# Kernel tuning notes

Hardware: AMD Instinct MI355X
Metric: run time of the kernel (lower is better)

The kernel has to match this reference:

```python
import jax, jax.numpy as jnp
import numpy as np

N, C, T, V, K = 32, 256, 64, 25, 3   # batch, in_channels, frames, joints, adjacency partitions
D = 256                               # out_channels
KT = 9                                # temporal kernel size
PAD = (KT - 1) // 2
EPS = 1e-5                            # BatchNorm eps (torch default)


def setup_inputs() -> dict:
    key = jax.random.key(0)
    ks = jax.random.split(key, 5)
    x = jax.random.normal(ks[0], (N, C, T, V), jnp.float32)
    A = jax.random.uniform(ks[1], (K, V, V), jnp.float32)           # learnable adjacency
    W_gcn = jax.random.normal(ks[2], (K, D, C), jnp.float32) * (2.0 / C) ** 0.5  # K stacked 1x1 convs
    b_gcn = jnp.zeros((K, D), jnp.float32)
    W_tcn = jax.random.normal(ks[3], (D, D, KT, 1), jnp.float32) * (2.0 / (D * KT)) ** 0.5  # kaiming fan_out
    b_tcn = jnp.zeros((D,), jnp.float32)
    gamma = jnp.ones((D,), jnp.float32)   # bn_init(bn, 1)
    beta = jnp.zeros((D,), jnp.float32)
    return dict(x=x, A=A, W_gcn=W_gcn, b_gcn=b_gcn, W_tcn=W_tcn,
                b_tcn=b_tcn, gamma=gamma, beta=beta)


def reference(x, A, W_gcn, b_gcn, W_tcn, b_tcn, gamma, beta):
    # ---- GCN: per-partition 1x1 conv over channels, then graph aggregation via A[k], summed over k ----
    # y[k,n,d,t,v] = sum_c W_gcn[k,d,c] * x[n,c,t,v] + b_gcn[k,d]
    y = jnp.einsum('kdc,nctv->kndtv', W_gcn, x) + b_gcn[:, None, :, None, None]
    # aggregate neighbors: sum_v y[k,n,d,t,v] * A[k,v,w], accumulated over partitions k
    y = jnp.einsum('kndtv,kvw->ndtw', y, A)        # [N, D, T, V]

    # ---- TCN: (9,1) temporal conv + BatchNorm2d (batch statistics) ----
    z = jax.lax.conv_general_dilated(
        y, W_tcn, window_strides=(1, 1), padding=((PAD, PAD), (0, 0)),
        dimension_numbers=('NCHW', 'OIHW', 'NCHW'))
    z = z + b_tcn[None, :, None, None]
    mean = jnp.mean(z, axis=(0, 2, 3), keepdims=True)
    var = jnp.mean((z - mean) ** 2, axis=(0, 2, 3), keepdims=True)  # biased, as torch BN training fwd
    z = gamma[None, :, None, None] * (z - mean) * jax.lax.rsqrt(var + EPS) + beta[None, :, None, None]

    # ---- residual (identity branch: in==out, stride==1) + ReLU ----
    return jax.nn.relu(z + x)
```

## Files before the change

### kernel.cpp

```cpp
#include <hip/hip_runtime.h>
#include <math.h>

typedef unsigned short u16;
typedef short v8s __attribute__((ext_vector_type(8)));
typedef float v4f __attribute__((ext_vector_type(4)));

#define AS1 __attribute__((address_space(1)))
#define AS3 __attribute__((address_space(3)))

__device__ __forceinline__ float bf2f(u16 u) {
    union { unsigned int i; float f; } c; c.i = ((unsigned int)u) << 16; return c.f;
}
__device__ __forceinline__ u16 f2bf(float f) {
    union { float f; unsigned int i; } c; c.f = f;
    unsigned int u = c.i;
    return (u16)((u + 0x7FFFu + ((u >> 16) & 1u)) >> 16);
}
__device__ __forceinline__ void gload_lds16(const void* g, void* l) {
    __builtin_amdgcn_global_load_lds((const AS1 void*)(uintptr_t)g,
                                     (AS3 void*)(unsigned int)(uintptr_t)l,
                                     16, 0, 0);
}

#define Nn 32
#define Tt 64
#define Vv 25
#define NP 51200
#define NBLK 400

__global__ __launch_bounds__(256) void prep_kernel(
    const float* __restrict__ Wg, const float* __restrict__ Wt,
    const float* __restrict__ A, const float* __restrict__ bg,
    u16* __restrict__ Wgb, u16* __restrict__ Wtb,
    float* __restrict__ bias2, float* __restrict__ zpad)
{
    const int idx = blockIdx.x * 256 + threadIdx.x;
    const int stride = gridDim.x * 256;
    for (int i = idx; i < 256 * 2304; i += stride) {
        int d = i / 2304, r = i - d * 2304, dt = r >> 8, c = r & 255;
        Wtb[i] = f2bf(Wt[(d * 256 + c) * 9 + dt]);
    }
    for (int i = idx; i < 256 * 768; i += stride) {
        int d = i / 768, r = i - d * 768, k = r >> 8, c = r & 255;
        Wgb[i] = f2bf(Wg[(k * 256 + d) * 256 + c]);
    }
    for (int i = idx; i < 25 * 256; i += stride) {
        int w = i >> 8, d = i & 255;
        float s = 0.f;
        for (int k = 0; k < 3; ++k) {
            float cs = 0.f;
            for (int v = 0; v < 25; ++v) cs += A[(k * 25 + v) * 25 + w];
            s += bg[k * 256 + d] * cs;
        }
        bias2[i] = s;
    }
    for (int i = idx; i < 256; i += stride) zpad[i] = 0.f;
}

__global__ __launch_bounds__(256) void xa_kernel(
    const float* __restrict__ x, const float* __restrict__ A,
    u16* __restrict__ xa2)
{
    const int t = blockIdx.x, n = blockIdx.y;
    const int tid = threadIdx.x;
    __shared__ float xs[256 * 25];

    for (int i = tid; i < 6400; i += 256) {
        int c = i / 25, v = i - c * 25;
        xs[i] = x[((n * 256 + c) * 64 + t) * 25 + v];
    }
    __syncthreads();

    float xr[25];
    #pragma unroll
    for (int v = 0; v < 25; ++v) xr[v] = xs[tid * 25 + v];

    const size_t pbase = ((size_t)n * 64 + t) * 25;
    #pragma unroll 1
    for (int k = 0; k < 3; ++k) {
        float o[25];
        #pragma unroll
        for (int w = 0; w < 25; ++w) {
            float acc = 0.f;
            #pragma unroll
            for (int v = 0; v < 25; ++v)
                acc = fmaf(xr[v], A[(k * 25 + v) * 25 + w], acc);
            o[w] = acc;
        }
        u16* dst = xa2 + k * 256 + tid;
        #pragma unroll
        for (int w = 0; w < 25; ++w)
            dst[(pbase + w) * 768] = f2bf(o[w]);
    }
}

template<int KTOT, bool TCN>
__global__ __launch_bounds__(512, 2) void gemm_kernel(
    const u16* __restrict__ Ad, const u16* __restrict__ Bw,
    const float* __restrict__ bias, u16* __restrict__ outB,
    float* __restrict__ psum, float* __restrict__ psq,
    const u16* __restrict__ zpad)
{
    __shared__ u16 smem[24576];
    u16* As = smem;
    u16* Bs = smem + 8192;

    const int tid = threadIdx.x;
    const int wid = tid >> 6, lane = tid & 63;
    const int lr = lane & 15, hk = lane >> 4;
    const int wm = wid >> 2, wn = wid & 3;
    const int blk = blockIdx.x;
    const int rA = lane >> 3, sA = lane & 7;

    v4f acc[4][4];
    const v4f vzero = {0.f, 0.f, 0.f, 0.f};
    #pragma unroll
    for (int mf = 0; mf < 4; ++mf)
        #pragma unroll
        for (int nf = 0; nf < 4; ++nf) acc[mf][nf] = vzero;

    for (int kt = 0; kt < KTOT / 64; ++kt) {
        #pragma unroll
        for (int i = 0; i < 2; ++i) {
            const int ch = wid + i * 8;
            const int row = ch * 8 + rA;
            const int p = blk * 128 + row;
            const int ss = sA ^ (row & 7);
            const u16* src;
            if (TCN) {
                const int dt = kt >> 2, c0 = (kt & 3) << 6;
                const int tv = p % 1600, t = tv / 25;
                const int tp = t + dt - 4;
                const int p2 = p + (dt - 4) * 25;
                src = ((unsigned)tp < 64u) ? (Ad + (size_t)p2 * 256 + c0 + ss * 8) : zpad;
            } else {
                src = Ad + (size_t)p * 768 + kt * 64 + ss * 8;
            }
            gload_lds16(src, (char*)As + ch * 1024);
        }
        #pragma unroll
        for (int i = 0; i < 4; ++i) {
            const int ch = wid + i * 8;
            const int d = ch * 8 + rA;
            const int ss = sA ^ (d & 7);
            gload_lds16(Bw + (size_t)d * KTOT + kt * 64 + ss * 8, (char*)Bs + ch * 1024);
        }
        __syncthreads();

        v8s a[4][2], b[4][2];
        #pragma unroll
        for (int mf = 0; mf < 4; ++mf)
            #pragma unroll
            for (int kk = 0; kk < 2; ++kk) {
                const int row = wm * 64 + mf * 16 + lr;
                const int slot = kk * 4 + hk;
                a[mf][kk] = *(const v8s*)((const char*)As + row * 128 + ((slot ^ (row & 7)) << 4));
            }
        #pragma unroll
        for (int nf = 0; nf < 4; ++nf)
            #pragma unroll
            for (int kk = 0; kk < 2; ++kk) {
                const int row = wn * 64 + nf * 16 + lr;
                const int slot = kk * 4 + hk;
                b[nf][kk] = *(const v8s*)((const char*)Bs + row * 128 + ((slot ^ (row & 7)) << 4));
            }
        #pragma unroll
        for (int kk = 0; kk < 2; ++kk)
            #pragma unroll
            for (int mf = 0; mf < 4; ++mf)
                #pragma unroll
                for (int nf = 0; nf < 4; ++nf)
                    acc[mf][nf] = __builtin_amdgcn_mfma_f32_16x16x32_bf16(
                        a[mf][kk], b[nf][kk], acc[mf][nf], 0, 0, 0);
        __syncthreads();
    }

    if (!TCN) {
        #pragma unroll
        for (int mf = 0; mf < 4; ++mf) {
            #pragma unroll
            for (int j = 0; j < 4; ++j) {
                const int p = blk * 128 + wm * 64 + mf * 16 + hk * 4 + j;
                const int w = p % 25;
                #pragma unroll
                for (int nf = 0; nf < 4; ++nf) {
                    const int d = wn * 64 + nf * 16 + lr;
                    outB[(size_t)p * 256 + d] = f2bf(acc[mf][nf][j] + bias[w * 256 + d]);
                }
            }
        }
    } else {
        float s[4], q[4];
        #pragma unroll
        for (int nf = 0; nf < 4; ++nf) {
            const int d = wn * 64 + nf * 16 + lr;
            const float bb = bias[d];
            s[nf] = 0.f; q[nf] = 0.f;
            #pragma unroll
            for (int mf = 0; mf < 4; ++mf) {
                #pragma unroll
                for (int j = 0; j < 4; ++j) {
                    const int p = blk * 128 + wm * 64 + mf * 16 + hk * 4 + j;
                    const float zz = acc[mf][nf][j] + bb;
                    outB[(size_t)p * 256 + d] = f2bf(zz);
                    s[nf] += zz; q[nf] += zz * zz;
                }
            }
            s[nf] += __shfl_xor(s[nf], 16); s[nf] += __shfl_xor(s[nf], 32);
            q[nf] += __shfl_xor(q[nf], 16); q[nf] += __shfl_xor(q[nf], 32);
        }
        __syncthreads();
        float* red = (float*)smem;
        if (hk == 0) {
            #pragma unroll
            for (int nf = 0; nf < 4; ++nf) {
                const int d = wn * 64 + nf * 16 + lr;
                red[wm * 256 + d] = s[nf];
                red[512 + wm * 256 + d] = q[nf];
            }
        }
        __syncthreads();
        if (tid < 256) {
            psum[(size_t)tid * NBLK + blk] = red[tid] + red[256 + tid];
            psq[(size_t)tid * NBLK + blk]  = red[512 + tid] + red[768 + tid];
        }
    }
}

__global__ __launch_bounds__(256) void bn_stats_kernel(
    const float* __restrict__ psum, const float* __restrict__ psq,
    const float* __restrict__ gamma, const float* __restrict__ beta,
    float* __restrict__ scale, float* __restrict__ shift)
{
    const int d = blockIdx.x, tid = threadIdx.x;
    float s = 0.f, q = 0.f;
    for (int i = tid; i < NBLK; i += 256) {
        s += psum[(size_t)d * NBLK + i];
        q += psq[(size_t)d * NBLK + i];
    }
    #pragma unroll
    for (int off = 32; off; off >>= 1) {
        s += __shfl_down(s, off);
        q += __shfl_down(q, off);
    }
    __shared__ float rs[4], rq[4];
    if ((tid & 63) == 0) { rs[tid >> 6] = s; rq[tid >> 6] = q; }
    __syncthreads();
    if (tid == 0) {
        s = rs[0] + rs[1] + rs[2] + rs[3];
        q = rq[0] + rq[1] + rq[2] + rq[3];
        const float mean = s / 51200.f;
        const float var = q / 51200.f - mean * mean;
        const float inv = rsqrtf(var + 1e-5f);
        scale[d] = gamma[d] * inv;
        shift[d] = beta[d] - gamma[d] * inv * mean;
    }
}

__global__ __launch_bounds__(256) void bn_apply_kernel(
    const u16* __restrict__ zb, const float* __restrict__ x,
    const float* __restrict__ scale, const float* __restrict__ shift,
    float* __restrict__ out)
{
    const int chunk = blockIdx.x;
    const int n = blockIdx.y;
    const int tid = threadIdx.x;
    __shared__ u16 zs[128 * 66];
    const size_t p0 = (size_t)n * 1600 + chunk * 64;

    for (int half = 0; half < 2; ++half) {
        const int d0 = half * 128;
        if (half) __syncthreads();
        for (int i = tid; i < 128 * 64; i += 256) {
            const int pl = i >> 7, dl = i & 127;
            zs[dl * 66 + pl] = zb[(p0 + pl) * 256 + d0 + dl];
        }
        __syncthreads();
        for (int i = tid; i < 128 * 64; i += 256) {
            const int dl = i >> 6, j = i & 63;
            const int d = d0 + dl;
            const size_t addr = ((size_t)n * 256 + d) * 1600 + chunk * 64 + j;
            const float r = bf2f(zs[dl * 66 + j]) * scale[d] + shift[d] + x[addr];
            out[addr] = fmaxf(r, 0.f);
        }
    }
}

extern "C" void kernel_launch(void* const* d_in, const int* in_sizes, int n_in,
                              void* d_out, int out_size, void* d_ws, size_t ws_size,
                              hipStream_t stream)
{
    const float* x     = (const float*)d_in[0];
    const float* A     = (const float*)d_in[1];
    const float* Wg    = (const float*)d_in[2];
    const float* bg    = (const float*)d_in[3];
    const float* Wt    = (const float*)d_in[4];
    const float* bt    = (const float*)d_in[5];
    const float* gamma = (const float*)d_in[6];
    const float* beta  = (const float*)d_in[7];
    float* out = (float*)d_out;

    char* w = (char*)d_ws;
    u16*   xa2   = (u16*)(w);
    u16*   y2T   = (u16*)(w + 78643200);
    u16*   zb    = (u16*)(w + 104857600);
    u16*   Wgb   = (u16*)(w + 131072000);
    u16*   Wtb   = (u16*)(w + 131465216);
    float* bias2 = (float*)(w + 132644864);
    float* psum  = (float*)(w + 132670464);
    float* psq   = (float*)(w + 133080064);
    float* scale = (float*)(w + 133489664);
    float* shift = (float*)(w + 133490688);
    float* zpad  = (float*)(w + 133491712);

    prep_kernel<<<512, 256, 0, stream>>>(Wg, Wt, A, bg, Wgb, Wtb, bias2, zpad);
    xa_kernel<<<dim3(64, 32), 256, 0, stream>>>(x, A, xa2);
    gemm_kernel<768, false><<<NBLK, 512, 0, stream>>>(xa2, Wgb, bias2, y2T,
                                                      nullptr, nullptr, (const u16*)zpad);
    gemm_kernel<2304, true><<<NBLK, 512, 0, stream>>>(y2T, Wtb, bt, zb,
                                                      psum, psq, (const u16*)zpad);
    bn_stats_kernel<<<256, 256, 0, stream>>>(psum, psq, gamma, beta, scale, shift);
    bn_apply_kernel<<<dim3(25, 32), 256, 0, stream>>>(zb, x, scale, shift, out);
}
```

Baseline: 169.8 us.

## Double-buffer GEMM LDS loads, shrink tile to 128x128, swizzle block order

The two GEMM kernels move from a 128x256 tile with 512 threads and a single LDS buffer to 128x128 tiles with 256 threads and two LDS buffers. Global-to-LDS loads for step k+2 are issued while step k computes, using explicit vmcnt waits and raw barriers. Launching 800 blocks with an XCD-aware swizzle is meant to improve occupancy and L2 reuse of the A rows across the two N-halves. The cost is that each A tile is now loaded twice, once per N-half, and the hand-placed waitcnt bookkeeping is fragile.

```diff
diff --git a/kernel.cpp b/kernel.cpp
--- a/kernel.cpp
+++ b/kernel.cpp
@@ -95,22 +95,25 @@
 }
 
 template<int KTOT, bool TCN>
-__global__ __launch_bounds__(512, 2) void gemm_kernel(
+__global__ __launch_bounds__(256, 2) void gemm_kernel(
     const u16* __restrict__ Ad, const u16* __restrict__ Bw,
     const float* __restrict__ bias, u16* __restrict__ outB,
     float* __restrict__ psum, float* __restrict__ psq,
     const u16* __restrict__ zpad)
 {
-    __shared__ u16 smem[24576];
-    u16* As = smem;
-    u16* Bs = smem + 8192;
+    constexpr int NT = KTOT / 64;
+    __shared__ u16 smem[2][16384];
 
     const int tid = threadIdx.x;
     const int wid = tid >> 6, lane = tid & 63;
     const int lr = lane & 15, hk = lane >> 4;
-    const int wm = wid >> 2, wn = wid & 3;
-    const int blk = blockIdx.x;
+    const int wm = wid >> 1, wn = wid & 1;
     const int rA = lane >> 3, sA = lane & 7;
+
+    const int orig = blockIdx.x;
+    const int swz = (orig & 7) * 100 + (orig >> 3);
+    const int nh = swz / 400, m = swz % 400;
+    const int d0 = nh * 128;
 
     v4f acc[4][4];
     const v4f vzero = {0.f, 0.f, 0.f, 0.f};
@@ -119,34 +122,41 @@
         #pragma unroll
         for (int nf = 0; nf < 4; ++nf) acc[mf][nf] = vzero;
 
-    for (int kt = 0; kt < KTOT / 64; ++kt) {
-        #pragma unroll
-        for (int i = 0; i < 2; ++i) {
-            const int ch = wid + i * 8;
-            const int row = ch * 8 + rA;
-            const int p = blk * 128 + row;
-            const int ss = sA ^ (row & 7);
-            const u16* src;
-            if (TCN) {
-                const int dt = kt >> 2, c0 = (kt & 3) << 6;
-                const int tv = p % 1600, t = tv / 25;
-                const int tp = t + dt - 4;
-                const int p2 = p + (dt - 4) * 25;
-                src = ((unsigned)tp < 64u) ? (Ad + (size_t)p2 * 256 + c0 + ss * 8) : zpad;
-            } else {
-                src = Ad + (size_t)p * 768 + kt * 64 + ss * 8;
-            }
-            gload_lds16(src, (char*)As + ch * 1024);
-        }
-        #pragma unroll
-        for (int i = 0; i < 4; ++i) {
-            const int ch = wid + i * 8;
-            const int d = ch * 8 + rA;
-            const int ss = sA ^ (d & 7);
-            gload_lds16(Bw + (size_t)d * KTOT + kt * 64 + ss * 8, (char*)Bs + ch * 1024);
-        }
-        __syncthreads();
-
+#define STAGE(buf, ktv)                                                        \
+    {                                                                          \
+        _Pragma("unroll")                                                      \
+        for (int i = 0; i < 4; ++i) {                                          \
+            const int ch = wid + i * 4;                                        \
+            const int row = ch * 8 + rA;                                       \
+            const int ss = sA ^ (row & 7);                                     \
+            const u16* srcA;                                                   \
+            if (TCN) {                                                         \
+                const int dt = (ktv) >> 2, c0 = ((ktv)&3) << 6;                \
+                const int p = m * 128 + row;                                   \
+                const int tv = p % 1600, t = tv / 25;                          \
+                const int tp = t + dt - 4;                                     \
+                srcA = ((unsigned)tp < 64u)                                    \
+                     ? (Ad + (size_t)(p + (dt - 4) * 25) * 256 + c0 + ss * 8)  \
+                     : zpad;                                                   \
+            } else {                                                           \
+                srcA = Ad + (size_t)(m * 128 + row) * 768 + (ktv)*64 + ss * 8; \
+            }                                                                  \
+            gload_lds16(srcA, (char*)&smem[buf][0] + ch * 1024);               \
+            gload_lds16(Bw + (size_t)(d0 + row) * KTOT + (ktv)*64 + ss * 8,    \
+                        (char*)&smem[buf][8192] + ch * 1024);                  \
+        }                                                                      \
+    }
+
+    STAGE(0, 0);
+    STAGE(1, 1);
+    asm volatile("s_waitcnt vmcnt(8)" ::: "memory");
+    __builtin_amdgcn_s_barrier();
+
+    #pragma unroll 2
+    for (int kt = 0; kt < NT; ++kt) {
+        const int cur = kt & 1;
+        const u16* As = &smem[cur][0];
+        const u16* Bs = &smem[cur][8192];
         v8s a[4][2], b[4][2];
         #pragma unroll
         for (int mf = 0; mf < 4; ++mf)
@@ -172,19 +182,28 @@
                 for (int nf = 0; nf < 4; ++nf)
                     acc[mf][nf] = __builtin_amdgcn_mfma_f32_16x16x32_bf16(
                         a[mf][kk], b[nf][kk], acc[mf][nf], 0, 0, 0);
-        __syncthreads();
-    }
+        __builtin_amdgcn_sched_barrier(0);
+        __builtin_amdgcn_s_barrier();
+        if (kt + 2 < NT) {
+            STAGE(cur, kt + 2);
+            asm volatile("s_waitcnt vmcnt(8)" ::: "memory");
+        } else {
+            asm volatile("s_waitcnt vmcnt(0)" ::: "memory");
+        }
+        __builtin_amdgcn_s_barrier();
+    }
+#undef STAGE
 
     if (!TCN) {
         #pragma unroll
         for (int mf = 0; mf < 4; ++mf) {
             #pragma unroll
             for (int j = 0; j < 4; ++j) {
-                const int p = blk * 128 + wm * 64 + mf * 16 + hk * 4 + j;
+                const int p = m * 128 + wm * 64 + mf * 16 + hk * 4 + j;
                 const int w = p % 25;
                 #pragma unroll
                 for (int nf = 0; nf < 4; ++nf) {
-                    const int d = wn * 64 + nf * 16 + lr;
+                    const int d = d0 + wn * 64 + nf * 16 + lr;
                     outB[(size_t)p * 256 + d] = f2bf(acc[mf][nf][j] + bias[w * 256 + d]);
                 }
             }
@@ -193,14 +212,14 @@
         float s[4], q[4];
         #pragma unroll
         for (int nf = 0; nf < 4; ++nf) {
-            const int d = wn * 64 + nf * 16 + lr;
+            const int d = d0 + wn * 64 + nf * 16 + lr;
             const float bb = bias[d];
             s[nf] = 0.f; q[nf] = 0.f;
             #pragma unroll
             for (int mf = 0; mf < 4; ++mf) {
                 #pragma unroll
                 for (int j = 0; j < 4; ++j) {
-                    const int p = blk * 128 + wm * 64 + mf * 16 + hk * 4 + j;
+                    const int p = m * 128 + wm * 64 + mf * 16 + hk * 4 + j;
                     const float zz = acc[mf][nf][j] + bb;
                     outB[(size_t)p * 256 + d] = f2bf(zz);
                     s[nf] += zz; q[nf] += zz * zz;
@@ -209,20 +228,19 @@
             s[nf] += __shfl_xor(s[nf], 16); s[nf] += __shfl_xor(s[nf], 32);
             q[nf] += __shfl_xor(q[nf], 16); q[nf] += __shfl_xor(q[nf], 32);
         }
+        float* red = (float*)&smem[0][0];
+        if (hk == 0) {
+            #pragma unroll
+            for (int nf = 0; nf < 4; ++nf) {
+                const int dl = wn * 64 + nf * 16 + lr;
+                red[wm * 128 + dl] = s[nf];
+                red[256 + wm * 128 + dl] = q[nf];
+            }
+        }
         __syncthreads();
-        float* red = (float*)smem;
-        if (hk == 0) {
-            #pragma unroll
-            for (int nf = 0; nf < 4; ++nf) {
-                const int d = wn * 64 + nf * 16 + lr;
-                red[wm * 256 + d] = s[nf];
-                red[512 + wm * 256 + d] = q[nf];
-            }
-        }
-        __syncthreads();
-        if (tid < 256) {
-            psum[(size_t)tid * NBLK + blk] = red[tid] + red[256 + tid];
-            psq[(size_t)tid * NBLK + blk]  = red[512 + tid] + red[768 + tid];
+        if (tid < 128) {
+            psum[(size_t)(d0 + tid) * NBLK + m] = red[tid] + red[128 + tid];
+            psq[(size_t)(d0 + tid) * NBLK + m]  = red[256 + tid] + red[384 + tid];
         }
     }
 }
@@ -315,10 +333,10 @@
 
     prep_kernel<<<512, 256, 0, stream>>>(Wg, Wt, A, bg, Wgb, Wtb, bias2, zpad);
     xa_kernel<<<dim3(64, 32), 256, 0, stream>>>(x, A, xa2);
-    gemm_kernel<768, false><<<NBLK, 512, 0, stream>>>(xa2, Wgb, bias2, y2T,
-                                                      nullptr, nullptr, (const u16*)zpad);
-    gemm_kernel<2304, true><<<NBLK, 512, 0, stream>>>(y2T, Wtb, bt, zb,
-                                                      psum, psq, (const u16*)zpad);
+    gemm_kernel<768, false><<<800, 256, 0, stream>>>(xa2, Wgb, bias2, y2T,
+                                                     nullptr, nullptr, (const u16*)zpad);
+    gemm_kernel<2304, true><<<800, 256, 0, stream>>>(y2T, Wtb, bt, zb,
+                                                     psum, psq, (const u16*)zpad);
     bn_stats_kernel<<<256, 256, 0, stream>>>(psum, psq, gamma, beta, scale, shift);
     bn_apply_kernel<<<dim3(25, 32), 256, 0, stream>>>(zb, x, scale, shift, out);
 }
```

Result: slower. 189.6 us (+11.7%).

## Double-buffer GEMM LDS tiles with 256-row blocks and interleaved prefetch

Applied to the files above, without the earlier changes.

Reworks the shared GEMM kernel to use 256x256 output tiles per block, which doubles the per-warp M fragments, and two LDS buffers. The next K-tile is prefetched with global_load_lds in chunks interleaved between MFMA groups, using setprio and sched_barrier, so only one barrier per K step remains. Block indices are remapped across XCDs and the number of stat partials is halved. This raises register and LDS use and drops the two-blocks-per-CU occupancy hint, and with 200 blocks only part of the CUs may be filled.

```diff
diff --git a/kernel.cpp b/kernel.cpp
--- a/kernel.cpp
+++ b/kernel.cpp
@@ -26,7 +26,7 @@
 #define Tt 64
 #define Vv 25
 #define NP 51200
-#define NBLK 400
+#define NBLK 200
 
 __global__ __launch_bounds__(256) void prep_kernel(
     const float* __restrict__ Wg, const float* __restrict__ Wt,
@@ -95,92 +95,143 @@
 }
 
 template<int KTOT, bool TCN>
-__global__ __launch_bounds__(512, 2) void gemm_kernel(
+__global__ __launch_bounds__(512) void gemm_kernel(
     const u16* __restrict__ Ad, const u16* __restrict__ Bw,
     const float* __restrict__ bias, u16* __restrict__ outB,
     float* __restrict__ psum, float* __restrict__ psq,
     const u16* __restrict__ zpad)
 {
-    __shared__ u16 smem[24576];
-    u16* As = smem;
-    u16* Bs = smem + 8192;
+    constexpr int NT = KTOT / 64;
+    __shared__ u16 smem[2][32768];
 
     const int tid = threadIdx.x;
     const int wid = tid >> 6, lane = tid & 63;
     const int lr = lane & 15, hk = lane >> 4;
     const int wm = wid >> 2, wn = wid & 3;
-    const int blk = blockIdx.x;
     const int rA = lane >> 3, sA = lane & 7;
 
-    v4f acc[4][4];
+    const int orig = blockIdx.x;
+    const int m = (orig & 7) * 25 + (orig >> 3);
+
+    v4f acc[8][4];
     const v4f vzero = {0.f, 0.f, 0.f, 0.f};
     #pragma unroll
-    for (int mf = 0; mf < 4; ++mf)
+    for (int mf = 0; mf < 8; ++mf)
         #pragma unroll
         for (int nf = 0; nf < 4; ++nf) acc[mf][nf] = vzero;
 
-    for (int kt = 0; kt < KTOT / 64; ++kt) {
-        #pragma unroll
-        for (int i = 0; i < 2; ++i) {
-            const int ch = wid + i * 8;
-            const int row = ch * 8 + rA;
-            const int p = blk * 128 + row;
-            const int ss = sA ^ (row & 7);
-            const u16* src;
-            if (TCN) {
-                const int dt = kt >> 2, c0 = (kt & 3) << 6;
-                const int tv = p % 1600, t = tv / 25;
-                const int tp = t + dt - 4;
-                const int p2 = p + (dt - 4) * 25;
-                src = ((unsigned)tp < 64u) ? (Ad + (size_t)p2 * 256 + c0 + ss * 8) : zpad;
-            } else {
-                src = Ad + (size_t)p * 768 + kt * 64 + ss * 8;
-            }
-            gload_lds16(src, (char*)As + ch * 1024);
-        }
-        #pragma unroll
-        for (int i = 0; i < 4; ++i) {
-            const int ch = wid + i * 8;
-            const int d = ch * 8 + rA;
-            const int ss = sA ^ (d & 7);
-            gload_lds16(Bw + (size_t)d * KTOT + kt * 64 + ss * 8, (char*)Bs + ch * 1024);
-        }
+#define STAGE2(bufp, ktv, i)                                                   \
+    {                                                                          \
+        const int ch = (i) * 8 + wid;                                          \
+        const int row = ch * 8 + rA;                                           \
+        const int ss = sA ^ rA;                               \
+        const u16* srcA;                                                       \
+        if (TCN) {                                                             \
+            const int dt = (ktv) >> 2, c0 = ((ktv)&3) << 6;                    \
+            const int p = m * 256 + row;                                       \
+            const int t = (p % 1600) / 25;                                     \
+            const int tp = t + dt - 4;                                         \
+            srcA = ((unsigned)tp < 64u)                                        \
+                 ? (Ad + (size_t)(p + (dt - 4) * 25) * 256 + c0 + ss * 8)      \
+                 : zpad;                                                       \
+        } else {                                                               \
+            srcA = Ad + (size_t)(m * 256 + row) * 768 + (ktv)*64 + ss * 8;     \
+        }                                                                      \
+        gload_lds16(srcA, (char*)(bufp) + ch * 1024);                          \
+        gload_lds16(Bw + (size_t)row * KTOT + (ktv)*64 + ss * 8,               \
+                    (char*)(bufp) + 32768 + ch * 1024);                        \
+    }
+
+#define LDA_(dst, mfv, kkv)                                                    \
+    {                                                                          \
+        const int row = wm * 128 + (mfv)*16 + lr;                              \
+        dst = *(const v8s*)((const char*)As + row * 128 +                      \
+                            ((((kkv)*4 + hk) ^ (row & 7)) << 4));              \
+    }
+#define LDB_(dst, nfv, kkv)                                                    \
+    {                                                                          \
+        const int row = wn * 64 + (nfv)*16 + lr;                               \
+        dst = *(const v8s*)((const char*)Bs + row * 128 +                      \
+                            ((((kkv)*4 + hk) ^ (row & 7)) << 4));              \
+    }
+
+    #pragma unroll
+    for (int i = 0; i < 4; ++i) STAGE2(&smem[0][0], 0, i);
+    __syncthreads();
+
+    #pragma unroll 1
+    for (int kt = 0; kt < NT; ++kt) {
+        const u16* As = &smem[kt & 1][0];
+        const u16* Bs = As + 16384;
+        u16* nbuf = &smem[(kt + 1) & 1][0];
+        const bool pf = (kt + 1 < NT);
+        v8s aL[4], aH[4], b0[4], b1[4];
+
+        if (pf) { STAGE2(nbuf, kt + 1, 0); STAGE2(nbuf, kt + 1, 1); }
+        #pragma unroll
+        for (int nf = 0; nf < 4; ++nf) LDB_(b0[nf], nf, 0);
+        #pragma unroll
+        for (int mf = 0; mf < 4; ++mf) LDA_(aL[mf], mf, 0);
+        __builtin_amdgcn_s_setprio(1);
+        #pragma unroll
+        for (int mf = 0; mf < 4; ++mf)
+            #pragma unroll
+            for (int nf = 0; nf < 4; ++nf)
+                acc[mf][nf] = __builtin_amdgcn_mfma_f32_16x16x32_bf16(
+                    aL[mf], b0[nf], acc[mf][nf], 0, 0, 0);
+        __builtin_amdgcn_s_setprio(0);
+        __builtin_amdgcn_sched_barrier(0);
+
+        if (pf) { STAGE2(nbuf, kt + 1, 2); STAGE2(nbuf, kt + 1, 3); }
+        #pragma unroll
+        for (int mf = 0; mf < 4; ++mf) LDA_(aH[mf], mf + 4, 0);
+        __builtin_amdgcn_s_setprio(1);
+        #pragma unroll
+        for (int mf = 0; mf < 4; ++mf)
+            #pragma unroll
+            for (int nf = 0; nf < 4; ++nf)
+                acc[mf + 4][nf] = __builtin_amdgcn_mfma_f32_16x16x32_bf16(
+                    aH[mf], b0[nf], acc[mf + 4][nf], 0, 0, 0);
+        __builtin_amdgcn_s_setprio(0);
+        __builtin_amdgcn_sched_barrier(0);
+
+        #pragma unroll
+        for (int nf = 0; nf < 4; ++nf) LDB_(b1[nf], nf, 1);
+        #pragma unroll
+        for (int mf = 0; mf < 4; ++mf) LDA_(aL[mf], mf, 1);
+        __builtin_amdgcn_s_setprio(1);
+        #pragma unroll
+        for (int mf = 0; mf < 4; ++mf)
+            #pragma unroll
+            for (int nf = 0; nf < 4; ++nf)
+                acc[mf][nf] = __builtin_amdgcn_mfma_f32_16x16x32_bf16(
+                    aL[mf], b1[nf], acc[mf][nf], 0, 0, 0);
+        __builtin_amdgcn_s_setprio(0);
+        __builtin_amdgcn_sched_barrier(0);
+
+        #pragma unroll
+        for (int mf = 0; mf < 4; ++mf) LDA_(aH[mf], mf + 4, 1);
+        __builtin_amdgcn_s_setprio(1);
+        #pragma unroll
+        for (int mf = 0; mf < 4; ++mf)
+            #pragma unroll
+            for (int nf = 0; nf < 4; ++nf)
+                acc[mf + 4][nf] = __builtin_amdgcn_mfma_f32_16x16x32_bf16(
+                    aH[mf], b1[nf], acc[mf + 4][nf], 0, 0, 0);
+        __builtin_amdgcn_s_setprio(0);
+
         __syncthreads();
-
-        v8s a[4][2], b[4][2];
-        #pragma unroll
-        for (int mf = 0; mf < 4; ++mf)
-            #pragma unroll
-            for (int kk = 0; kk < 2; ++kk) {
-                const int row = wm * 64 + mf * 16 + lr;
-                const int slot = kk * 4 + hk;
-                a[mf][kk] = *(const v8s*)((const char*)As + row * 128 + ((slot ^ (row & 7)) << 4));
-            }
-        #pragma unroll
-        for (int nf = 0; nf < 4; ++nf)
-            #pragma unroll
-            for (int kk = 0; kk < 2; ++kk) {
-                const int row = wn * 64 + nf * 16 + lr;
-                const int slot = kk * 4 + hk;
-                b[nf][kk] = *(const v8s*)((const char*)Bs + row * 128 + ((slot ^ (row & 7)) << 4));
-            }
-        #pragma unroll
-        for (int kk = 0; kk < 2; ++kk)
-            #pragma unroll
-            for (int mf = 0; mf < 4; ++mf)
-                #pragma unroll
-                for (int nf = 0; nf < 4; ++nf)
-                    acc[mf][nf] = __builtin_amdgcn_mfma_f32_16x16x32_bf16(
-                        a[mf][kk], b[nf][kk], acc[mf][nf], 0, 0, 0);
-        __syncthreads();
-    }
+    }
+#undef STAGE2
+#undef LDA_
+#undef LDB_
 
     if (!TCN) {
         #pragma unroll
-        for (int mf = 0; mf < 4; ++mf) {
+        for (int mf = 0; mf < 8; ++mf) {
             #pragma unroll
             for (int j = 0; j < 4; ++j) {
-                const int p = blk * 128 + wm * 64 + mf * 16 + hk * 4 + j;
+                const int p = m * 256 + wm * 128 + mf * 16 + hk * 4 + j;
                 const int w = p % 25;
                 #pragma unroll
                 for (int nf = 0; nf < 4; ++nf) {
@@ -197,10 +248,10 @@
             const float bb = bias[d];
             s[nf] = 0.f; q[nf] = 0.f;
             #pragma unroll
-            for (int mf = 0; mf < 4; ++mf) {
+            for (int mf = 0; mf < 8; ++mf) {
                 #pragma unroll
                 for (int j = 0; j < 4; ++j) {
-                    const int p = blk * 128 + wm * 64 + mf * 16 + hk * 4 + j;
+                    const int p = m * 256 + wm * 128 + mf * 16 + hk * 4 + j;
                     const float zz = acc[mf][nf][j] + bb;
                     outB[(size_t)p * 256 + d] = f2bf(zz);
                     s[nf] += zz; q[nf] += zz * zz;
@@ -210,7 +261,7 @@
             q[nf] += __shfl_xor(q[nf], 16); q[nf] += __shfl_xor(q[nf], 32);
         }
         __syncthreads();
-        float* red = (float*)smem;
+        float* red = (float*)&smem[0][0];
         if (hk == 0) {
             #pragma unroll
             for (int nf = 0; nf < 4; ++nf) {
@@ -221,8 +272,8 @@
         }
         __syncthreads();
         if (tid < 256) {
-            psum[(size_t)tid * NBLK + blk] = red[tid] + red[256 + tid];
-            psq[(size_t)tid * NBLK + blk]  = red[512 + tid] + red[768 + tid];
+            psum[(size_t)tid * NBLK + m] = red[tid] + red[256 + tid];
+            psq[(size_t)tid * NBLK + m]  = red[512 + tid] + red[768 + tid];
         }
     }
 }
```

Measured after the change: 167.3 us. Within noise of the previous version (-1.5%).

## Split GEMM output columns into two 128-wide halves with XCD-aware block swizzle

Applied to the files above, without the earlier changes.

Each GEMM block now computes a 128x128 output tile instead of 128x256. The grid doubles to 800 blocks, and block IDs are remapped so that blocks on the same XCD share M tiles. This raises parallelism and cuts per-thread accumulator registers, which could allow more occupancy. In exchange, the A tile is loaded twice, once per N half, and the launch-bounds minimum-block hint is dropped.

```diff
diff --git a/kernel.cpp b/kernel.cpp
--- a/kernel.cpp
+++ b/kernel.cpp
@@ -95,59 +95,61 @@
 }
 
 template<int KTOT, bool TCN>
-__global__ __launch_bounds__(512, 2) void gemm_kernel(
+__global__ __launch_bounds__(512) void gemm_kernel(
     const u16* __restrict__ Ad, const u16* __restrict__ Bw,
     const float* __restrict__ bias, u16* __restrict__ outB,
     float* __restrict__ psum, float* __restrict__ psq,
     const u16* __restrict__ zpad)
 {
-    __shared__ u16 smem[24576];
-    u16* As = smem;
-    u16* Bs = smem + 8192;
+    constexpr int NT = KTOT / 64;
+    __shared__ u16 smem[16384];
 
     const int tid = threadIdx.x;
     const int wid = tid >> 6, lane = tid & 63;
     const int lr = lane & 15, hk = lane >> 4;
     const int wm = wid >> 2, wn = wid & 3;
-    const int blk = blockIdx.x;
     const int rA = lane >> 3, sA = lane & 7;
 
-    v4f acc[4][4];
+    const int orig = blockIdx.x;
+    const int swz = (orig & 7) * 100 + (orig >> 3);
+    const int nh = swz / 400, m = swz % 400;
+    const int d0 = nh * 128;
+
+    u16* As = smem;
+    u16* Bs = smem + 8192;
+
+    v4f acc[4][2];
     const v4f vzero = {0.f, 0.f, 0.f, 0.f};
     #pragma unroll
     for (int mf = 0; mf < 4; ++mf)
         #pragma unroll
-        for (int nf = 0; nf < 4; ++nf) acc[mf][nf] = vzero;
-
-    for (int kt = 0; kt < KTOT / 64; ++kt) {
+        for (int nf = 0; nf < 2; ++nf) acc[mf][nf] = vzero;
+
+    for (int kt = 0; kt < NT; ++kt) {
         #pragma unroll
         for (int i = 0; i < 2; ++i) {
             const int ch = wid + i * 8;
             const int row = ch * 8 + rA;
-            const int p = blk * 128 + row;
-            const int ss = sA ^ (row & 7);
-            const u16* src;
+            const int ss = sA ^ rA;
+            const u16* srcA;
             if (TCN) {
                 const int dt = kt >> 2, c0 = (kt & 3) << 6;
-                const int tv = p % 1600, t = tv / 25;
+                const int p = m * 128 + row;
+                const int t = (p % 1600) / 25;
                 const int tp = t + dt - 4;
-                const int p2 = p + (dt - 4) * 25;
-                src = ((unsigned)tp < 64u) ? (Ad + (size_t)p2 * 256 + c0 + ss * 8) : zpad;
+                srcA = ((unsigned)tp < 64u)
+                     ? (Ad + (size_t)(p + (dt - 4) * 25) * 256 + c0 + ss * 8)
+                     : zpad;
             } else {
-                src = Ad + (size_t)p * 768 + kt * 64 + ss * 8;
-            }
-            gload_lds16(src, (char*)As + ch * 1024);
-        }
-        #pragma unroll
-        for (int i = 0; i < 4; ++i) {
-            const int ch = wid + i * 8;
-            const int d = ch * 8 + rA;
-            const int ss = sA ^ (d & 7);
-            gload_lds16(Bw + (size_t)d * KTOT + kt * 64 + ss * 8, (char*)Bs + ch * 1024);
+                srcA = Ad + (size_t)(m * 128 + row) * 768 + kt * 64 + ss * 8;
+            }
+            gload_lds16(srcA, (char*)As + ch * 1024);
+            gload_lds16(Bw + (size_t)(d0 + row) * KTOT + kt * 64 + ss * 8,
+                        (char*)Bs + ch * 1024);
         }
         __syncthreads();
 
-        v8s a[4][2], b[4][2];
+        v8s a[4][2], b[2][2];
         #pragma unroll
         for (int mf = 0; mf < 4; ++mf)
             #pragma unroll
@@ -157,10 +159,10 @@
                 a[mf][kk] = *(const v8s*)((const char*)As + row * 128 + ((slot ^ (row & 7)) << 4));
             }
         #pragma unroll
-        for (int nf = 0; nf < 4; ++nf)
+        for (int nf = 0; nf < 2; ++nf)
             #pragma unroll
             for (int kk = 0; kk < 2; ++kk) {
-                const int row = wn * 64 + nf * 16 + lr;
+                const int row = wn * 32 + nf * 16 + lr;
                 const int slot = kk * 4 + hk;
                 b[nf][kk] = *(const v8s*)((const char*)Bs + row * 128 + ((slot ^ (row & 7)) << 4));
             }
@@ -169,7 +171,7 @@
             #pragma unroll
             for (int mf = 0; mf < 4; ++mf)
                 #pragma unroll
-                for (int nf = 0; nf < 4; ++nf)
+                for (int nf = 0; nf < 2; ++nf)
                     acc[mf][nf] = __builtin_amdgcn_mfma_f32_16x16x32_bf16(
                         a[mf][kk], b[nf][kk], acc[mf][nf], 0, 0, 0);
         __syncthreads();
@@ -180,27 +182,27 @@
         for (int mf = 0; mf < 4; ++mf) {
             #pragma unroll
             for (int j = 0; j < 4; ++j) {
-                const int p = blk * 128 + wm * 64 + mf * 16 + hk * 4 + j;
+                const int p = m * 128 + wm * 64 + mf * 16 + hk * 4 + j;
                 const int w = p % 25;
                 #pragma unroll
-                for (int nf = 0; nf < 4; ++nf) {
-                    const int d = wn * 64 + nf * 16 + lr;
+                for (int nf = 0; nf < 2; ++nf) {
+                    const int d = d0 + wn * 32 + nf * 16 + lr;
                     outB[(size_t)p * 256 + d] = f2bf(acc[mf][nf][j] + bias[w * 256 + d]);
                 }
             }
         }
     } else {
-        float s[4], q[4];
-        #pragma unroll
-        for (int nf = 0; nf < 4; ++nf) {
-            const int d = wn * 64 + nf * 16 + lr;
+        float s[2], q[2];
+        #pragma unroll
+        for (int nf = 0; nf < 2; ++nf) {
+            const int d = d0 + wn * 32 + nf * 16 + lr;
             const float bb = bias[d];
             s[nf] = 0.f; q[nf] = 0.f;
             #pragma unroll
             for (int mf = 0; mf < 4; ++mf) {
                 #pragma unroll
                 for (int j = 0; j < 4; ++j) {
-                    const int p = blk * 128 + wm * 64 + mf * 16 + hk * 4 + j;
+                    const int p = m * 128 + wm * 64 + mf * 16 + hk * 4 + j;
                     const float zz = acc[mf][nf][j] + bb;
                     outB[(size_t)p * 256 + d] = f2bf(zz);
                     s[nf] += zz; q[nf] += zz * zz;
@@ -209,20 +211,19 @@
             s[nf] += __shfl_xor(s[nf], 16); s[nf] += __shfl_xor(s[nf], 32);
             q[nf] += __shfl_xor(q[nf], 16); q[nf] += __shfl_xor(q[nf], 32);
         }
-        __syncthreads();
         float* red = (float*)smem;
         if (hk == 0) {
             #pragma unroll
-            for (int nf = 0; nf < 4; ++nf) {
-                const int d = wn * 64 + nf * 16 + lr;
-                red[wm * 256 + d] = s[nf];
-                red[512 + wm * 256 + d] = q[nf];
+            for (int nf = 0; nf < 2; ++nf) {
+                const int dl = wn * 32 + nf * 16 + lr;
+                red[wm * 128 + dl] = s[nf];
+                red[256 + wm * 128 + dl] = q[nf];
             }
         }
         __syncthreads();
-        if (tid < 256) {
-            psum[(size_t)tid * NBLK + blk] = red[tid] + red[256 + tid];
-            psq[(size_t)tid * NBLK + blk]  = red[512 + tid] + red[768 + tid];
+        if (tid < 128) {
+            psum[(size_t)(d0 + tid) * NBLK + m] = red[tid] + red[128 + tid];
+            psq[(size_t)(d0 + tid) * NBLK + m]  = red[256 + tid] + red[384 + tid];
         }
     }
 }
@@ -315,10 +316,10 @@
 
     prep_kernel<<<512, 256, 0, stream>>>(Wg, Wt, A, bg, Wgb, Wtb, bias2, zpad);
     xa_kernel<<<dim3(64, 32), 256, 0, stream>>>(x, A, xa2);
-    gemm_kernel<768, false><<<NBLK, 512, 0, stream>>>(xa2, Wgb, bias2, y2T,
-                                                      nullptr, nullptr, (const u16*)zpad);
-    gemm_kernel<2304, true><<<NBLK, 512, 0, stream>>>(y2T, Wtb, bt, zb,
-                                                      psum, psq, (const u16*)zpad);
+    gemm_kernel<768, false><<<800, 512, 0, stream>>>(xa2, Wgb, bias2, y2T,
+                                                     nullptr, nullptr, (const u16*)zpad);
+    gemm_kernel<2304, true><<<800, 512, 0, stream>>>(y2T, Wtb, bt, zb,
+                                                     psum, psq, (const u16*)zpad);
     bn_stats_kernel<<<256, 256, 0, stream>>>(psum, psq, gamma, beta, scale, shift);
     bn_apply_kernel<<<dim3(25, 32), 256, 0, stream>>>(zb, x, scale, shift, out);
 }
```

After: 197.2 us. +16.2%, slower.
